# Kernel optimization log

Measured on AMD Instinct MI355X. Metric: run time of the kernel, lower is better.

The kernel has to match this reference:

```python
import jax, jax.numpy as jnp
import numpy as np

E = 1024      # embedding_size
H = 16        # num_head
DQ = DK = DV = 64  # per-head q/k/v size


def setup_inputs() -> dict:
    key = jax.random.key(0)
    ks = jax.random.split(key, 9)
    B, S = 2, 2048
    s = 1.0 / np.sqrt(E)
    return {
        "q": jax.random.normal(ks[0], (B, S, E), jnp.float32),
        "k": jax.random.normal(ks[1], (B, S, E), jnp.float32),
        "v": jax.random.normal(ks[2], (B, S, E), jnp.float32),
        "w_q": jax.random.normal(ks[3], (E, H * DQ), jnp.float32) * s,
        "b_q": jax.random.normal(ks[4], (H * DQ,), jnp.float32) * s,
        "w_k": jax.random.normal(ks[5], (E, H * DK), jnp.float32) * s,
        "b_k": jax.random.normal(ks[6], (H * DK,), jnp.float32) * s,
        "w_v": jax.random.normal(ks[7], (E, H * DV), jnp.float32) * s,
        "b_v": jax.random.normal(ks[8], (H * DV,), jnp.float32) * s,
    }


def reference(q, k, v, w_q, b_q, w_k, b_k, w_v, b_v):
    B, Sq, _ = q.shape
    Sk = k.shape[1]
    # projections -> [B, S, H, d] -> [B, H, S, d]
    qh = (q @ w_q + b_q).reshape(B, Sq, H, DQ).transpose(0, 2, 1, 3)
    kh = (k @ w_k + b_k).reshape(B, Sk, H, DK).transpose(0, 2, 1, 3)
    vh = (v @ w_v + b_v).reshape(B, Sk, H, DV).transpose(0, 2, 1, 3)
    # scaled dot-product attention; scores [B, H, Sq, Sk]
    scores = jnp.einsum("bhqd,bhkd->bhqk", qh, kh) / jnp.sqrt(jnp.float32(DQ))
    weights = jax.nn.softmax(scores, axis=-1)
    out = jnp.einsum("bhqk,bhkd->bhqd", weights, vh)  # [B, H, Sq, DV]
    return out.transpose(0, 2, 1, 3).reshape(B, Sq, H * DV)
```

## Files before the change

### kernel.cpp

```cpp
#include <hip/hip_runtime.h>
#include <hip/hip_bf16.h>

typedef __bf16 bf16_t;
typedef bf16_t bf16x8 __attribute__((ext_vector_type(8)));
typedef bf16_t bf16x4 __attribute__((ext_vector_type(4)));
typedef short  short4v __attribute__((ext_vector_type(4)));
typedef float  f32x4  __attribute__((ext_vector_type(4)));

#define MFMA16(a,b,c) __builtin_amdgcn_mfma_f32_16x16x32_bf16(a, b, c, 0, 0, 0)

constexpr int S = 2048, H = 16, Dh = 64;
constexpr int N = H * Dh;
constexpr int K = 1024;
constexpr float QSCALE = 0.125f * 1.4426950408889634f;

static __device__ inline void load_lds16(const bf16_t* g, bf16_t* l) {
  __builtin_amdgcn_global_load_lds(
      (const __attribute__((address_space(1))) void*)g,
      (__attribute__((address_space(3))) void*)l, 16, 0, 0);
}

static __device__ inline ushort f2bb(float x) {
  bf16_t h = (bf16_t)x;
  return __builtin_bit_cast(ushort, h);
}

__global__ __launch_bounds__(256) void prep(
    const float* __restrict__ q, const float* __restrict__ k,
    const float* __restrict__ v,
    const float* __restrict__ wq, const float* __restrict__ wk,
    const float* __restrict__ wv,
    bf16_t* __restrict__ xq, bf16_t* __restrict__ xk, bf16_t* __restrict__ xv,
    bf16_t* __restrict__ wtq, bf16_t* __restrict__ wtk, bf16_t* __restrict__ wtv) {
  __shared__ ushort tile[64][68];
  int bx = blockIdx.x, t = threadIdx.x;
  if (bx < 6144) {
    int z = bx >> 11, bb = bx & 2047;
    const float* xi = z == 0 ? q : z == 1 ? k : v;
    bf16_t*      xo = z == 0 ? xq : z == 1 ? xk : xv;
    size_t idx = ((size_t)bb * 256 + t) * 8;
    float4 a = *(const float4*)&xi[idx];
    float4 b = *(const float4*)&xi[idx + 4];
    bf16x8 w;
    w[0] = (bf16_t)a.x; w[1] = (bf16_t)a.y; w[2] = (bf16_t)a.z; w[3] = (bf16_t)a.w;
    w[4] = (bf16_t)b.x; w[5] = (bf16_t)b.y; w[6] = (bf16_t)b.z; w[7] = (bf16_t)b.w;
    *(bf16x8*)&xo[idx] = w;
  } else {
    int zz = bx - 6144;
    int z = zz >> 8, bb = zz & 255;
    const float* wi = z == 0 ? wq : z == 1 ? wk : wv;
    ushort*      wo = (ushort*)(z == 0 ? wtq : z == 1 ? wtk : wtv);
    int k0 = (bb >> 4) * 64, n0 = (bb & 15) * 64;
    for (int i = 0; i < 4; ++i) {
      int idx4 = (i * 256 + t) * 4;
      int r = idx4 >> 6, c = idx4 & 63;
      float4 vv = *(const float4*)&wi[(size_t)(k0 + r) * N + n0 + c];
      tile[r][c] = f2bb(vv.x); tile[r][c + 1] = f2bb(vv.y);
      tile[r][c + 2] = f2bb(vv.z); tile[r][c + 3] = f2bb(vv.w);
    }
    __syncthreads();
    for (int i = 0; i < 4; ++i) {
      int idx4 = (i * 256 + t) * 4;
      int r = idx4 >> 6, c = idx4 & 63;
      ushort4 vv;
      vv.x = tile[c][r]; vv.y = tile[c + 1][r];
      vv.z = tile[c + 2][r]; vv.w = tile[c + 3][r];
      *(ushort4*)&wo[(size_t)(n0 + r) * K + k0 + c] = vv;
    }
  }
}

__global__ __launch_bounds__(256) void proj_gemm(
    const bf16_t* __restrict__ xq, const bf16_t* __restrict__ xk,
    const bf16_t* __restrict__ xv,
    const bf16_t* __restrict__ wtq, const bf16_t* __restrict__ wtk,
    const bf16_t* __restrict__ wtv,
    const float* __restrict__ bq, const float* __restrict__ bk,
    const float* __restrict__ bv,
    bf16_t* __restrict__ qh, bf16_t* __restrict__ kh, bf16_t* __restrict__ vt) {
  int mode = blockIdx.z;
  const bf16_t* X  = mode == 0 ? xq  : mode == 1 ? xk  : wtv;
  const bf16_t* Wt = mode == 0 ? wtq : mode == 1 ? wtk : xv;
  const float*  Bi = mode == 0 ? bq  : mode == 1 ? bk  : bv;

  __shared__ __align__(16) bf16_t smem[17408];
  bf16_t (*Ash)[64] = (bf16_t(*)[64])smem;
  bf16_t (*Bsh)[64] = (bf16_t(*)[64])(smem + 8192);
  bf16_t* Cs = smem;

  int tid = threadIdx.x;
  int wave = tid >> 6, lane = tid & 63;
  int lr = lane & 15, lg = lane >> 4;
  int lrow = lane >> 3, lchunk = lane & 7;
  int m0 = (mode < 2 ? blockIdx.y : blockIdx.x) * 128;
  int n0 = (mode < 2 ? blockIdx.x : blockIdx.y) * 128;
  int wm = (wave >> 1) * 64, wn = (wave & 1) * 64;

  f32x4 acc[4][4];
  for (int i = 0; i < 4; ++i)
    for (int j = 0; j < 4; ++j) acc[i][j] = (f32x4){0.f, 0.f, 0.f, 0.f};

  for (int ko = 0; ko < K / 64; ++ko) {
    __syncthreads();
    for (int j = 0; j < 4; ++j) {
      int r = wave * 32 + j * 8 + lrow;
      int gc = (lchunk ^ (r & 7)) * 8;
      load_lds16(&X [(size_t)(m0 + r) * K + ko * 64 + gc], &Ash[r][lchunk * 8]);
      load_lds16(&Wt[(size_t)(n0 + r) * K + ko * 64 + gc], &Bsh[r][lchunk * 8]);
    }
    __syncthreads();
    for (int kk = 0; kk < 2; ++kk) {
      bf16x8 af[4], bfr[4];
      for (int i = 0; i < 4; ++i) {
        int rr = wm + i * 16 + lr;
        af[i] = *(const bf16x8*)&Ash[rr][(((kk << 2) | lg) ^ (rr & 7)) * 8];
      }
      for (int j = 0; j < 4; ++j) {
        int rr = wn + j * 16 + lr;
        bfr[j] = *(const bf16x8*)&Bsh[rr][(((kk << 2) | lg) ^ (rr & 7)) * 8];
      }
      for (int i = 0; i < 4; ++i)
        for (int j = 0; j < 4; ++j)
          acc[i][j] = MFMA16(af[i], bfr[j], acc[i][j]);
    }
  }

  float badd[4][4][4];
  if (mode < 2) {
    float bvv[4];
    for (int j = 0; j < 4; ++j) bvv[j] = Bi[n0 + wn + j * 16 + lr];
    for (int i = 0; i < 4; ++i)
      for (int j = 0; j < 4; ++j)
        for (int r = 0; r < 4; ++r) badd[i][j][r] = bvv[j];
  } else {
    for (int i = 0; i < 4; ++i)
      for (int r = 0; r < 4; ++r) {
        float bm = Bi[m0 + wm + i * 16 + lg * 4 + r];
        for (int j = 0; j < 4; ++j) badd[i][j][r] = bm;
      }
  }

  __syncthreads();
  for (int i = 0; i < 4; ++i)
    for (int j = 0; j < 4; ++j)
      for (int r = 0; r < 4; ++r) {
        float vvv = acc[i][j][r] + badd[i][j][r];
        if (mode == 0) vvv *= QSCALE;
        Cs[(size_t)(wm + i * 16 + lg * 4 + r) * 136 + wn + j * 16 + lr] = (bf16_t)vvv;
      }
  __syncthreads();

  bf16_t* o = mode == 0 ? qh : mode == 1 ? kh : vt;
  for (int p = 0; p < 8; ++p) {
    int idx = p * 256 + tid;
    int row = idx >> 4, ch = idx & 15;
    bf16x8 vv = *(const bf16x8*)&Cs[(size_t)row * 136 + ch * 8];
    size_t dst;
    if (mode < 2) {
      int m_g = m0 + row, n_g = n0 + ch * 8;
      int b = m_g >> 11, s = m_g & 2047;
      int h = n_g >> 6, d = n_g & 63;
      dst = (((size_t)(b * 16 + h) * 2048) + s) * 64 + d;
    } else {
      int w_g = m0 + row, t_g = n0 + ch * 8;
      int b = t_g >> 11, s = t_g & 2047;
      dst = ((size_t)(b * 1024 + w_g)) * 2048 + s;
    }
    *(uint4*)&o[dst] = __builtin_bit_cast(uint4, vv);
  }
}

__global__ __launch_bounds__(512, 2) void attn(
    const bf16_t* __restrict__ qh, const bf16_t* __restrict__ kh,
    const bf16_t* __restrict__ vt, float* __restrict__ out) {
  __shared__ __align__(16) bf16_t smem[16640];

  int tid = threadIdx.x, wave = tid >> 6, lane = tid & 63;
  int lr = lane & 15, lg = lane >> 4;
  int half = wave >> 2, w4 = wave & 3;
  int bh = blockIdx.y;
  int q0 = blockIdx.x * 128 + w4 * 32;

  bf16_t* kt = smem + half * 8192;
  bf16_t* vs = kt + 4096;

  const bf16_t* qg = qh + (size_t)bh * S * Dh;
  const bf16_t* kg = kh + (size_t)bh * S * Dh;
  const bf16_t* vg = vt + (size_t)bh * Dh * S;

  bf16x8 bqf[2][2];
#pragma unroll
  for (int ms = 0; ms < 2; ++ms)
#pragma unroll
    for (int kk = 0; kk < 2; ++kk)
      bqf[ms][kk] = *(const bf16x8*)
          &qg[(size_t)(q0 + ms * 16 + lr) * 64 + kk * 32 + lg * 8];

  bf16x8 ones8;
#pragma unroll
  for (int j = 0; j < 8; ++j) ones8[j] = (bf16_t)1.0f;

  f32x4 o_acc[2][4], lacc[2];
#pragma unroll
  for (int ms = 0; ms < 2; ++ms) {
    lacc[ms] = (f32x4){0.f, 0.f, 0.f, 0.f};
#pragma unroll
    for (int dt = 0; dt < 4; ++dt) o_acc[ms][dt] = (f32x4){0.f, 0.f, 0.f, 0.f};
  }

  int lrow = lane >> 3, lchunk = lane & 7;
  int srow0 = w4 * 16 + lrow;
  int srow1 = srow0 + 8;
  int sgc = (lchunk ^ (srow0 & 7)) * 8;
  int ld0 = srow0 * 64 + lchunk * 8;
  int ld1 = ld0 + 512;

  int cb = half * (S / 2);

  uint4 kr0 = *(const uint4*)&kg[(size_t)(cb + srow0) * 64 + sgc];
  uint4 kr1 = *(const uint4*)&kg[(size_t)(cb + srow1) * 64 + sgc];
  uint4 vr0 = *(const uint4*)&vg[(size_t)srow0 * S + cb + sgc];
  uint4 vr1 = *(const uint4*)&vg[(size_t)srow1 * S + cb + sgc];

  int sw = lr & 7, p4 = (lg & 1) * 4;

  constexpr int NITH = (S / 2) / 64;
  for (int it = 0; it < NITH; ++it) {
    __syncthreads();
    *(uint4*)&kt[ld0] = kr0;
    *(uint4*)&kt[ld1] = kr1;
    *(uint4*)&vs[ld0] = vr0;
    *(uint4*)&vs[ld1] = vr1;
    if (it + 1 < NITH) {
      int sk1 = cb + (it + 1) * 64;
      kr0 = *(const uint4*)&kg[(size_t)(sk1 + srow0) * 64 + sgc];
      kr1 = *(const uint4*)&kg[(size_t)(sk1 + srow1) * 64 + sgc];
      vr0 = *(const uint4*)&vg[(size_t)srow0 * S + sk1 + sgc];
      vr1 = *(const uint4*)&vg[(size_t)srow1 * S + sk1 + sgc];
    }
    __syncthreads();

    bf16x8 pa8[2][2];
#pragma unroll
    for (int tp = 0; tp < 2; ++tp) {
      f32x4 st[2][2];
#pragma unroll
      for (int ms = 0; ms < 2; ++ms)
#pragma unroll
        for (int ts = 0; ts < 2; ++ts) st[ms][ts] = (f32x4){0.f, 0.f, 0.f, 0.f};
#pragma unroll
      for (int ts = 0; ts < 2; ++ts) {
        int t = tp * 2 + ts;
        const bf16_t* krow = &kt[(t * 16 + lr) * 64];
        bf16x8 ak0 = *(const bf16x8*)&krow[(lg ^ sw) * 8];
        bf16x8 ak1 = *(const bf16x8*)&krow[((4 + lg) ^ sw) * 8];
#pragma unroll
        for (int ms = 0; ms < 2; ++ms) {
          st[ms][ts] = MFMA16(ak0, bqf[ms][0], st[ms][ts]);
          st[ms][ts] = MFMA16(ak1, bqf[ms][1], st[ms][ts]);
        }
      }
#pragma unroll
      for (int ms = 0; ms < 2; ++ms)
#pragma unroll
        for (int r = 0; r < 4; ++r) {
          pa8[ms][tp][r]     = (bf16_t)__builtin_amdgcn_exp2f(st[ms][0][r]);
          pa8[ms][tp][r + 4] = (bf16_t)__builtin_amdgcn_exp2f(st[ms][1][r]);
        }
    }

#pragma unroll
    for (int tp = 0; tp < 2; ++tp) {
      int g0 = tp * 4 + (lg >> 1);
#pragma unroll
      for (int dt = 0; dt < 4; ++dt) {
        const bf16_t* vrow = &vs[(dt * 16 + lr) * 64];
        bf16x4 lo = *(const bf16x4*)&vrow[((g0      ^ sw) * 8) + p4];
        bf16x4 hi = *(const bf16x4*)&vrow[(((g0 + 2) ^ sw) * 8) + p4];
        bf16x8 bb;
#pragma unroll
        for (int j = 0; j < 4; ++j) { bb[j] = lo[j]; bb[j + 4] = hi[j]; }
#pragma unroll
        for (int ms = 0; ms < 2; ++ms)
          o_acc[ms][dt] = MFMA16(pa8[ms][tp], bb, o_acc[ms][dt]);
      }
#pragma unroll
      for (int ms = 0; ms < 2; ++ms)
        lacc[ms] = MFMA16(pa8[ms][tp], ones8, lacc[ms]);
    }
  }

  __syncthreads();
  float* mo = (float*)smem;
  float* ls = mo + 8 * 16 * 64;

  if (half == 1) {
#pragma unroll
    for (int ms = 0; ms < 2; ++ms)
#pragma unroll
      for (int r = 0; r < 4; ++r) {
        int row = (w4 * 2 + ms) * 16 + lg * 4 + r;
#pragma unroll
        for (int dt = 0; dt < 4; ++dt)
          mo[row * 64 + dt * 16 + lr] = o_acc[ms][dt][r];
        if (lr == 0) ls[row] = lacc[ms][r];
      }
  }
  __syncthreads();
  if (half == 0) {
    int b = bh >> 4, hh = bh & 15;
#pragma unroll
    for (int ms = 0; ms < 2; ++ms)
#pragma unroll
      for (int r = 0; r < 4; ++r) {
        int row = (w4 * 2 + ms) * 16 + lg * 4 + r;
        float inv = 1.f / (lacc[ms][r] + ls[row]);
        int s_row = q0 + ms * 16 + lg * 4 + r;
        size_t base = ((size_t)(b * S + s_row)) * 1024 + hh * 64;
#pragma unroll
        for (int dt = 0; dt < 4; ++dt)
          out[base + dt * 16 + lr] =
              (o_acc[ms][dt][r] + mo[row * 64 + dt * 16 + lr]) * inv;
      }
  }
}

extern "C" void kernel_launch(void* const* d_in, const int* in_sizes, int n_in,
                              void* d_out, int out_size, void* d_ws, size_t ws_size,
                              hipStream_t stream) {
  const float* q  = (const float*)d_in[0];
  const float* k  = (const float*)d_in[1];
  const float* v  = (const float*)d_in[2];
  const float* wq = (const float*)d_in[3];
  const float* bq = (const float*)d_in[4];
  const float* wk = (const float*)d_in[5];
  const float* bk = (const float*)d_in[6];
  const float* wv = (const float*)d_in[7];
  const float* bv = (const float*)d_in[8];

  bf16_t* ws  = (bf16_t*)d_ws;
  constexpr size_t MW = (size_t)1 << 20;
  constexpr size_t MX = (size_t)4096 * 1024;
  bf16_t* wtq = ws;
  bf16_t* wtk = wtq + MW;
  bf16_t* wtv = wtk + MW;
  bf16_t* xq  = wtv + MW;
  bf16_t* xk  = xq + MX;
  bf16_t* xv  = xk + MX;
  bf16_t* qhd = xv + MX;
  bf16_t* khd = qhd + MX;
  bf16_t* vtd = khd + MX;
  float* out  = (float*)d_out;

  prep<<<6912, 256, 0, stream>>>(q, k, v, wq, wk, wv,
                                 xq, xk, xv, wtq, wtk, wtv);
  proj_gemm<<<dim3(8, 32, 3), 256, 0, stream>>>(xq, xk, xv, wtq, wtk, wtv,
                                                bq, bk, bv, qhd, khd, vtd);
  attn<<<dim3(16, 32), 512, 0, stream>>>(qhd, khd, vtd, out);
}
```

Baseline: 199.5 us.

## Double-buffer K/V tiles in LDS and remap attention block IDs for locality

The attention kernel now keeps two LDS buffers for the K and V tiles. It writes the next tile into the alternate buffer while the current one is being consumed, which removes one __syncthreads per iteration. The 2D grid is flattened into a 1D launch with a swizzled block-to-(head, q-tile) mapping, presumably to group blocks that share the same head's K/V across XCDs for cache reuse. LDS use grows to 64KB per block, which may limit occupancy at two blocks per CU.

```diff
diff --git a/kernel.cpp b/kernel.cpp
--- a/kernel.cpp
+++ b/kernel.cpp
@@ -173,16 +173,18 @@
 __global__ __launch_bounds__(512, 2) void attn(
     const bf16_t* __restrict__ qh, const bf16_t* __restrict__ kh,
     const bf16_t* __restrict__ vt, float* __restrict__ out) {
-  __shared__ __align__(16) bf16_t smem[16640];
+  __shared__ __align__(16) bf16_t smem[32768];
 
   int tid = threadIdx.x, wave = tid >> 6, lane = tid & 63;
   int lr = lane & 15, lg = lane >> 4;
   int half = wave >> 2, w4 = wave & 3;
-  int bh = blockIdx.y;
-  int q0 = blockIdx.x * 128 + w4 * 32;
-
-  bf16_t* kt = smem + half * 8192;
-  bf16_t* vs = kt + 4096;
+
+  int bid = blockIdx.x;
+  int logical = (bid & 7) * 64 + (bid >> 3);
+  int bh = logical >> 4;
+  int q0 = (logical & 15) * 128 + w4 * 32;
+
+  bf16_t* kt0 = smem + half * 8192;
 
   const bf16_t* qg = qh + (size_t)bh * S * Dh;
   const bf16_t* kg = kh + (size_t)bh * S * Dh;
@@ -221,24 +223,39 @@
   uint4 kr1 = *(const uint4*)&kg[(size_t)(cb + srow1) * 64 + sgc];
   uint4 vr0 = *(const uint4*)&vg[(size_t)srow0 * S + cb + sgc];
   uint4 vr1 = *(const uint4*)&vg[(size_t)srow1 * S + cb + sgc];
+  *(uint4*)&kt0[ld0] = kr0;
+  *(uint4*)&kt0[ld1] = kr1;
+  *(uint4*)&kt0[4096 + ld0] = vr0;
+  *(uint4*)&kt0[4096 + ld1] = vr1;
+  {
+    int sk1 = cb + 64;
+    kr0 = *(const uint4*)&kg[(size_t)(sk1 + srow0) * 64 + sgc];
+    kr1 = *(const uint4*)&kg[(size_t)(sk1 + srow1) * 64 + sgc];
+    vr0 = *(const uint4*)&vg[(size_t)srow0 * S + sk1 + sgc];
+    vr1 = *(const uint4*)&vg[(size_t)srow1 * S + sk1 + sgc];
+  }
 
   int sw = lr & 7, p4 = (lg & 1) * 4;
 
   constexpr int NITH = (S / 2) / 64;
   for (int it = 0; it < NITH; ++it) {
     __syncthreads();
-    *(uint4*)&kt[ld0] = kr0;
-    *(uint4*)&kt[ld1] = kr1;
-    *(uint4*)&vs[ld0] = vr0;
-    *(uint4*)&vs[ld1] = vr1;
     if (it + 1 < NITH) {
-      int sk1 = cb + (it + 1) * 64;
-      kr0 = *(const uint4*)&kg[(size_t)(sk1 + srow0) * 64 + sgc];
-      kr1 = *(const uint4*)&kg[(size_t)(sk1 + srow1) * 64 + sgc];
-      vr0 = *(const uint4*)&vg[(size_t)srow0 * S + sk1 + sgc];
-      vr1 = *(const uint4*)&vg[(size_t)srow1 * S + sk1 + sgc];
-    }
-    __syncthreads();
+      int wb = ((it + 1) & 1) * 16384;
+      *(uint4*)&kt0[wb + ld0] = kr0;
+      *(uint4*)&kt0[wb + ld1] = kr1;
+      *(uint4*)&kt0[wb + 4096 + ld0] = vr0;
+      *(uint4*)&kt0[wb + 4096 + ld1] = vr1;
+      if (it + 2 < NITH) {
+        int sk = cb + (it + 2) * 64;
+        kr0 = *(const uint4*)&kg[(size_t)(sk + srow0) * 64 + sgc];
+        kr1 = *(const uint4*)&kg[(size_t)(sk + srow1) * 64 + sgc];
+        vr0 = *(const uint4*)&vg[(size_t)srow0 * S + sk + sgc];
+        vr1 = *(const uint4*)&vg[(size_t)srow1 * S + sk + sgc];
+      }
+    }
+    const bf16_t* ktr = kt0 + (it & 1) * 16384;
+    const bf16_t* vsr = ktr + 4096;
 
     bf16x8 pa8[2][2];
 #pragma unroll
@@ -251,7 +268,7 @@
 #pragma unroll
       for (int ts = 0; ts < 2; ++ts) {
         int t = tp * 2 + ts;
-        const bf16_t* krow = &kt[(t * 16 + lr) * 64];
+        const bf16_t* krow = &ktr[(t * 16 + lr) * 64];
         bf16x8 ak0 = *(const bf16x8*)&krow[(lg ^ sw) * 8];
         bf16x8 ak1 = *(const bf16x8*)&krow[((4 + lg) ^ sw) * 8];
 #pragma unroll
@@ -274,7 +291,7 @@
       int g0 = tp * 4 + (lg >> 1);
 #pragma unroll
       for (int dt = 0; dt < 4; ++dt) {
-        const bf16_t* vrow = &vs[(dt * 16 + lr) * 64];
+        const bf16_t* vrow = &vsr[(dt * 16 + lr) * 64];
         bf16x4 lo = *(const bf16x4*)&vrow[((g0      ^ sw) * 8) + p4];
         bf16x4 hi = *(const bf16x4*)&vrow[(((g0 + 2) ^ sw) * 8) + p4];
         bf16x8 bb;
@@ -356,5 +373,5 @@
                                  xq, xk, xv, wtq, wtk, wtv);
   proj_gemm<<<dim3(8, 32, 3), 256, 0, stream>>>(xq, xk, xv, wtq, wtk, wtv,
                                                 bq, bk, bv, qhd, khd, vtd);
-  attn<<<dim3(16, 32), 512, 0, stream>>>(qhd, khd, vtd, out);
-}
+  attn<<<512, 512, 0, stream>>>(qhd, khd, vtd, out);
+}
```

After: 200.8 us. No clear change (+0.6%).
